# Kernel tuning notes

Hardware: AMD Instinct MI355X
Metric: run time of the kernel (lower is better)

The kernel has to match this reference:

```python
import jax, jax.numpy as jnp
import numpy as np
import math

B, S, D, H = 4, 2048, 512, 8
HD = D // H  # head dim = 64

def setup_inputs() -> dict:
    key = jax.random.key(0)
    ks = jax.random.split(key, 12)
    inp = {
        'queries': jax.random.normal(ks[0], (B, S, D), jnp.float32),
        'keys': jax.random.normal(ks[1], (B, S, D), jnp.float32),
        'values': jax.random.normal(ks[2], (B, S, D), jnp.float32),
        'valid_lens': jax.random.randint(ks[3], (B,), 0, 2048, jnp.int32),
        'Wq': jax.random.normal(ks[4], (D, D), jnp.float32) / math.sqrt(D),
        'bq': jnp.zeros((D,), jnp.float32),
        'Wk': jax.random.normal(ks[5], (D, D), jnp.float32) / math.sqrt(D),
        'bk': jnp.zeros((D,), jnp.float32),
        'Wv': jax.random.normal(ks[6], (D, D), jnp.float32) / math.sqrt(D),
        'bv': jnp.zeros((D,), jnp.float32),
        'Wo': jax.random.normal(ks[7], (D, D), jnp.float32) / math.sqrt(D),
        'bo': jnp.zeros((D,), jnp.float32),
    }
    return inp

def reference(queries, keys, values, valid_lens, Wq, bq, Wk, bk, Wv, bv, Wo, bo):
    # project and split heads: [B,S,D] -> [B,H,S,HD]
    def split_heads(x):
        return x.reshape(B, S, H, HD).transpose(0, 2, 1, 3)
    q = split_heads(queries @ Wq + bq)
    k = split_heads(keys @ Wk + bk)
    v = split_heads(values @ Wv + bv)
    # scores [B,H,Sq,Sk]
    scores = jnp.einsum('bhqd,bhkd->bhqk', q, k) / math.sqrt(HD)
    # masked softmax: mask key positions >= valid_len with -1e6 (d2l semantics)
    mask = jnp.arange(S)[None, None, None, :] < valid_lens[:, None, None, None]
    scores = jnp.where(mask, scores, -1e6)
    attn = jax.nn.softmax(scores, axis=-1)
    out = jnp.einsum('bhqk,bhkd->bhqd', attn, v)  # [B,H,S,HD]
    out = out.transpose(0, 2, 1, 3).reshape(B, S, D)
    return out @ Wo + bo
```

## Files before the change

### kernel.cpp

```cpp
#include <hip/hip_runtime.h>
#include <hip/hip_bf16.h>

typedef _Float16 half8 __attribute__((ext_vector_type(8)));
typedef _Float16 half4 __attribute__((ext_vector_type(4)));
typedef float floatx4 __attribute__((ext_vector_type(4)));

#define LOG2E 1.44269504088896340736f

__device__ __forceinline__ half8 cvt8(const float* p) {
    floatx4 a = *(const floatx4*)p;
    floatx4 b = *(const floatx4*)(p + 4);
    half8 h;
    h[0] = (_Float16)a[0]; h[1] = (_Float16)a[1]; h[2] = (_Float16)a[2]; h[3] = (_Float16)a[3];
    h[4] = (_Float16)b[0]; h[5] = (_Float16)b[1]; h[6] = (_Float16)b[2]; h[7] = (_Float16)b[3];
    return h;
}

__global__ __launch_bounds__(256) void transpose_w_kernel(
        const float* __restrict__ Wq, const float* __restrict__ Wk,
        const float* __restrict__ Wv, const float* __restrict__ Wo,
        _Float16* __restrict__ out) {
    const float* W = (blockIdx.z == 0) ? Wq : (blockIdx.z == 1) ? Wk : (blockIdx.z == 2) ? Wv : Wo;
    _Float16* o = out + (size_t)blockIdx.z * 512 * 512;
    __shared__ __align__(16) _Float16 t[64][72];
    int r0 = blockIdx.x * 64, c0 = blockIdx.y * 64;
    int tid = threadIdx.x;
    for (int i = 0; i < 2; i++) {
        int f = i * 256 + tid;
        int row = f >> 3, seg = f & 7;
        *(half8*)&t[row][seg * 8] = cvt8(W + (size_t)(r0 + row) * 512 + c0 + seg * 8);
    }
    __syncthreads();
    for (int i = 0; i < 2; i++) {
        int f = i * 256 + tid;
        int crow = f >> 3, seg = f & 7;
        half8 hv;
        for (int j = 0; j < 8; j++) hv[j] = t[seg * 8 + j][crow];
        *(half8*)(o + (size_t)(c0 + crow) * 512 + r0 + seg * 8) = hv;
    }
}

__global__ __launch_bounds__(256) void gemm_qkv_kernel(
        const float* __restrict__ Xq, const float* __restrict__ Xk, const float* __restrict__ Xv,
        const _Float16* __restrict__ WTall,
        const float* __restrict__ bq, const float* __restrict__ bk, const float* __restrict__ bv,
        _Float16* __restrict__ qo, _Float16* __restrict__ ko2, _Float16* __restrict__ vto) {
    int z = blockIdx.z;
    const float* X = (z == 0) ? Xq : (z == 1) ? Xk : Xv;
    const _Float16* BT = WTall + (size_t)z * 512 * 512;
    const float* bias = (z == 0) ? bq : (z == 1) ? bk : bv;

    __shared__ __align__(16) _Float16 Asm[128][72];
    __shared__ __align__(16) _Float16 Bsm[128][72];

    int tid = threadIdx.x;
    int wave = tid >> 6, lane = tid & 63;
    int lrow = lane & 15, quad = lane >> 4;
    int m0 = (wave >> 1) * 64, n0 = (wave & 1) * 64;
    int mBase = blockIdx.x * 128, nBase = blockIdx.y * 128;

    const floatx4 fz = {0.f, 0.f, 0.f, 0.f};
    floatx4 acc[4][4];
    for (int i = 0; i < 4; i++) for (int j = 0; j < 4; j++) acc[i][j] = fz;

    for (int kb = 0; kb < 512; kb += 64) {
        for (int i = 0; i < 4; i++) {
            int f = i * 256 + tid;
            int row = f >> 3, seg = f & 7;
            *(half8*)&Asm[row][seg * 8] = cvt8(X + (size_t)(mBase + row) * 512 + kb + seg * 8);
            *(half8*)&Bsm[row][seg * 8] = *(const half8*)(BT + (size_t)(nBase + row) * 512 + kb + seg * 8);
        }
        __syncthreads();
        for (int kc = 0; kc < 2; kc++) {
            int ko_ = kc * 32 + quad * 8;
            half8 a[4], b[4];
            for (int mt = 0; mt < 4; mt++) a[mt] = *(const half8*)&Asm[m0 + mt * 16 + lrow][ko_];
            for (int nt = 0; nt < 4; nt++) b[nt] = *(const half8*)&Bsm[n0 + nt * 16 + lrow][ko_];
            for (int mt = 0; mt < 4; mt++)
                for (int nt = 0; nt < 4; nt++)
                    acc[mt][nt] = __builtin_amdgcn_mfma_f32_16x16x32_f16(a[mt], b[nt], acc[mt][nt], 0, 0, 0);
        }
        __syncthreads();
    }

    if (z == 2) {
        for (int nt = 0; nt < 4; nt++) {
            int gc = nBase + n0 + nt * 16 + lrow;
            float bb = bias[gc];
            int h = gc >> 6, hd = gc & 63;
            for (int mt = 0; mt < 4; mt++) {
                int gr = mBase + m0 + mt * 16 + quad * 4;
                int b_ = gr >> 11, s = gr & 2047;
                half4 hv;
                for (int r = 0; r < 4; r++) hv[r] = (_Float16)(acc[mt][nt][r] + bb);
                *(half4*)(vto + (((size_t)(b_ * 8 + h) * 64 + hd) * 2048 + s)) = hv;
            }
        }
    } else {
        _Float16* out = (z == 0) ? qo : ko2;
        for (int nt = 0; nt < 4; nt++) {
            int gc = nBase + n0 + nt * 16 + lrow;
            float bb = bias[gc];
            int h = gc >> 6, hd = gc & 63;
            for (int mt = 0; mt < 4; mt++) {
                for (int r = 0; r < 4; r++) {
                    int gr = mBase + m0 + mt * 16 + quad * 4 + r;
                    int b_ = gr >> 11, s = gr & 2047;
                    out[(((size_t)b_ * 8 + h) * 2048 + s) * 64 + hd] = (_Float16)(acc[mt][nt][r] + bb);
                }
            }
        }
    }
}

__global__ __launch_bounds__(256) void attn_kernel(
        const _Float16* __restrict__ qws, const _Float16* __restrict__ kws, const _Float16* __restrict__ vtws,
        const int* __restrict__ vlens, _Float16* __restrict__ aout) {
    int idx = blockIdx.x;
    int b = ((idx & 3) + (idx >> 8)) & 3;
    int h = (idx >> 2) & 7;
    int q0 = ((idx >> 5) & 31) * 64;
    int bh = b * 8 + h;
    int L = vlens[b];
    bool uni = (L == 0);
    int nkt = uni ? 32 : ((L + 63) >> 6);
    int tid = threadIdx.x;
    int wave = tid >> 6, lane = tid & 63;
    int lrow = lane & 15, quad = lane >> 4;

    __shared__ __align__(16) _Float16 ksm[64][72];
    __shared__ __align__(16) _Float16 vtsm[80][72];

    for (int i = tid; i < 15 * 36; i += 256) {
        int r = i / 36, c = i % 36;
        ((float*)&vtsm[65 + r][0])[c] = 0.0f;
    }
    if (tid < 64) vtsm[64][tid] = (_Float16)1.0f;

    const _Float16* qbase = qws + ((size_t)bh * 2048 + q0) * 64;
    const _Float16* kbase = kws + (size_t)bh * 2048 * 64;
    const _Float16* vtbase = vtws + (size_t)bh * 64 * 2048;

    half8 qf[2];
    for (int kc = 0; kc < 2; kc++)
        qf[kc] = *(const half8*)(qbase + (wave * 16 + lrow) * 64 + kc * 32 + quad * 8);

    const floatx4 fz = {0.f, 0.f, 0.f, 0.f};
    floatx4 oacc[5];
    for (int nt = 0; nt < 5; nt++) oacc[nt] = fz;
    const float cexp = 0.125f * LOG2E;

    for (int kt = 0; kt < nkt; kt++) {
        const _Float16* ktile = kbase + (size_t)kt * 64 * 64;
        const _Float16* vttile = vtbase + kt * 64;
        for (int i = 0; i < 2; i++) {
            int f = i * 256 + tid;
            int row = f >> 3, seg = f & 7;
            *(half8*)&ksm[row][seg * 8] = *(const half8*)(ktile + f * 8);
            *(half8*)&vtsm[row][seg * 8] = *(const half8*)(vttile + (size_t)row * 2048 + seg * 8);
        }
        __syncthreads();

        floatx4 sacc[4];
        for (int km = 0; km < 4; km++) sacc[km] = fz;
        for (int kc = 0; kc < 2; kc++) {
            int ko_ = kc * 32 + quad * 8;
            for (int km = 0; km < 4; km++) {
                half8 kf = *(const half8*)&ksm[km * 16 + lrow][ko_];
                sacc[km] = __builtin_amdgcn_mfma_f32_16x16x32_f16(kf, qf[kc], sacc[km], 0, 0, 0);
            }
        }

        half4 pf[4];
        int kb0 = kt * 64 + quad * 4;
        for (int km = 0; km < 4; km++) {
            int kb = kb0 + km * 16;
            for (int r = 0; r < 4; r++) {
                float p = uni ? 1.0f : ((kb + r < L) ? exp2f(sacc[km][r] * cexp) : 0.0f);
                pf[km][r] = (_Float16)p;
            }
        }

        for (int km = 0; km < 4; km++) {
            int kk = km * 16 + quad * 4;
            for (int nt = 0; nt < 5; nt++) {
                half4 bvf = *(const half4*)&vtsm[nt * 16 + lrow][kk];
                oacc[nt] = __builtin_amdgcn_mfma_f32_16x16x16f16(pf[km], bvf, oacc[nt], 0, 0, 0);
            }
        }
        __syncthreads();
    }

    float inv[4];
    for (int r = 0; r < 4; r++)
        inv[r] = 1.0f / __shfl(oacc[4][r], quad << 4, 64);

    for (int nt = 0; nt < 4; nt++) {
        for (int r = 0; r < 4; r++) {
            int s = q0 + wave * 16 + quad * 4 + r;
            aout[((size_t)b * 2048 + s) * 512 + h * 64 + nt * 16 + lrow] =
                (_Float16)(oacc[nt][r] * inv[r]);
        }
    }
}

__global__ __launch_bounds__(256) void gemm_out_kernel(
        const _Float16* __restrict__ A, const _Float16* __restrict__ BT,
        const float* __restrict__ bias, float* __restrict__ out) {
    __shared__ __align__(16) _Float16 Asm[128][72];
    __shared__ __align__(16) _Float16 Bsm[128][72];

    int tid = threadIdx.x;
    int wave = tid >> 6, lane = tid & 63;
    int lrow = lane & 15, quad = lane >> 4;
    int m0 = (wave >> 1) * 64, n0 = (wave & 1) * 64;
    int mBase = blockIdx.x * 128, nBase = blockIdx.y * 128;

    const floatx4 fz = {0.f, 0.f, 0.f, 0.f};
    floatx4 acc[4][4];
    for (int i = 0; i < 4; i++) for (int j = 0; j < 4; j++) acc[i][j] = fz;

    for (int kb = 0; kb < 512; kb += 64) {
        for (int i = 0; i < 4; i++) {
            int f = i * 256 + tid;
            int row = f >> 3, seg = f & 7;
            *(half8*)&Asm[row][seg * 8] = *(const half8*)(A + (size_t)(mBase + row) * 512 + kb + seg * 8);
            *(half8*)&Bsm[row][seg * 8] = *(const half8*)(BT + (size_t)(nBase + row) * 512 + kb + seg * 8);
        }
        __syncthreads();
        for (int kc = 0; kc < 2; kc++) {
            int ko_ = kc * 32 + quad * 8;
            half8 a[4], b[4];
            for (int mt = 0; mt < 4; mt++) a[mt] = *(const half8*)&Asm[m0 + mt * 16 + lrow][ko_];
            for (int nt = 0; nt < 4; nt++) b[nt] = *(const half8*)&Bsm[n0 + nt * 16 + lrow][ko_];
            for (int mt = 0; mt < 4; mt++)
                for (int nt = 0; nt < 4; nt++)
                    acc[mt][nt] = __builtin_amdgcn_mfma_f32_16x16x32_f16(a[mt], b[nt], acc[mt][nt], 0, 0, 0);
        }
        __syncthreads();
    }

    for (int nt = 0; nt < 4; nt++) {
        int gc = nBase + n0 + nt * 16 + lrow;
        float bb = bias[gc];
        for (int mt = 0; mt < 4; mt++) {
            for (int r = 0; r < 4; r++) {
                int gr = mBase + m0 + mt * 16 + quad * 4 + r;
                out[(size_t)gr * 512 + gc] = acc[mt][nt][r] + bb;
            }
        }
    }
}

extern "C" void kernel_launch(void* const* d_in, const int* in_sizes, int n_in,
                              void* d_out, int out_size, void* d_ws, size_t ws_size,
                              hipStream_t stream) {
    const float* Q  = (const float*)d_in[0];
    const float* K  = (const float*)d_in[1];
    const float* V  = (const float*)d_in[2];
    const int*   VL = (const int*)d_in[3];
    const float* Wq = (const float*)d_in[4];
    const float* bq = (const float*)d_in[5];
    const float* Wk = (const float*)d_in[6];
    const float* bk = (const float*)d_in[7];
    const float* Wv = (const float*)d_in[8];
    const float* bv = (const float*)d_in[9];
    const float* Wo = (const float*)d_in[10];
    const float* bo = (const float*)d_in[11];

    char* ws = (char*)d_ws;
    _Float16* WT   = (_Float16*)ws;
    _Float16* qws  = (_Float16*)(ws + (size_t)(2)  * 1024 * 1024);
    _Float16* kws  = (_Float16*)(ws + (size_t)(10) * 1024 * 1024);
    _Float16* aout = (_Float16*)(ws + (size_t)(18) * 1024 * 1024);
    _Float16* vtws = (_Float16*)(ws + (size_t)(26) * 1024 * 1024);

    transpose_w_kernel<<<dim3(8, 8, 4), 256, 0, stream>>>(Wq, Wk, Wv, Wo, WT);
    gemm_qkv_kernel<<<dim3(64, 4, 3), 256, 0, stream>>>(Q, K, V, WT, bq, bk, bv, qws, kws, vtws);
    attn_kernel<<<dim3(1024, 1, 1), 256, 0, stream>>>(qws, kws, vtws, VL, aout);
    gemm_out_kernel<<<dim3(64, 4, 1), 256, 0, stream>>>(aout, WT + (size_t)3 * 512 * 512, bo, (float*)d_out);
}
```

Baseline: 206.9 us.

## Register-prefetch next tiles in GEMM and attention loops; fold softmax scale into Q

```diff
diff --git a/kernel.cpp b/kernel.cpp
--- a/kernel.cpp
+++ b/kernel.cpp
@@ -7,9 +7,7 @@
 
 #define LOG2E 1.44269504088896340736f
 
-__device__ __forceinline__ half8 cvt8(const float* p) {
-    floatx4 a = *(const floatx4*)p;
-    floatx4 b = *(const floatx4*)(p + 4);
+__device__ __forceinline__ half8 cvt8r(floatx4 a, floatx4 b) {
     half8 h;
     h[0] = (_Float16)a[0]; h[1] = (_Float16)a[1]; h[2] = (_Float16)a[2]; h[3] = (_Float16)a[3];
     h[4] = (_Float16)b[0]; h[5] = (_Float16)b[1]; h[6] = (_Float16)b[2]; h[7] = (_Float16)b[3];
@@ -28,7 +26,8 @@
     for (int i = 0; i < 2; i++) {
         int f = i * 256 + tid;
         int row = f >> 3, seg = f & 7;
-        *(half8*)&t[row][seg * 8] = cvt8(W + (size_t)(r0 + row) * 512 + c0 + seg * 8);
+        const float* p = W + (size_t)(r0 + row) * 512 + c0 + seg * 8;
+        *(half8*)&t[row][seg * 8] = cvt8r(*(const floatx4*)p, *(const floatx4*)(p + 4));
     }
     __syncthreads();
     for (int i = 0; i < 2; i++) {
@@ -63,14 +62,33 @@
     floatx4 acc[4][4];
     for (int i = 0; i < 4; i++) for (int j = 0; j < 4; j++) acc[i][j] = fz;
 
+    floatx4 areg[4][2];
+    half8 breg[4];
+    int srow[4], sseg[4];
+    for (int i = 0; i < 4; i++) { int f = i * 256 + tid; srow[i] = f >> 3; sseg[i] = f & 7; }
+
+    for (int i = 0; i < 4; i++) {
+        const float* pa = X + (size_t)(mBase + srow[i]) * 512 + sseg[i] * 8;
+        areg[i][0] = *(const floatx4*)pa;
+        areg[i][1] = *(const floatx4*)(pa + 4);
+        breg[i] = *(const half8*)(BT + (size_t)(nBase + srow[i]) * 512 + sseg[i] * 8);
+    }
+
     for (int kb = 0; kb < 512; kb += 64) {
         for (int i = 0; i < 4; i++) {
-            int f = i * 256 + tid;
-            int row = f >> 3, seg = f & 7;
-            *(half8*)&Asm[row][seg * 8] = cvt8(X + (size_t)(mBase + row) * 512 + kb + seg * 8);
-            *(half8*)&Bsm[row][seg * 8] = *(const half8*)(BT + (size_t)(nBase + row) * 512 + kb + seg * 8);
-        }
-        __syncthreads();
+            *(half8*)&Asm[srow[i]][sseg[i] * 8] = cvt8r(areg[i][0], areg[i][1]);
+            *(half8*)&Bsm[srow[i]][sseg[i] * 8] = breg[i];
+        }
+        __syncthreads();
+        if (kb + 64 < 512) {
+            int kn = kb + 64;
+            for (int i = 0; i < 4; i++) {
+                const float* pa = X + (size_t)(mBase + srow[i]) * 512 + kn + sseg[i] * 8;
+                areg[i][0] = *(const floatx4*)pa;
+                areg[i][1] = *(const floatx4*)(pa + 4);
+                breg[i] = *(const half8*)(BT + (size_t)(nBase + srow[i]) * 512 + kn + sseg[i] * 8);
+            }
+        }
         for (int kc = 0; kc < 2; kc++) {
             int ko_ = kc * 32 + quad * 8;
             half8 a[4], b[4];
@@ -142,24 +160,41 @@
     const _Float16* vtbase = vtws + (size_t)bh * 64 * 2048;
 
     half8 qf[2];
-    for (int kc = 0; kc < 2; kc++)
+    for (int kc = 0; kc < 2; kc++) {
         qf[kc] = *(const half8*)(qbase + (wave * 16 + lrow) * 64 + kc * 32 + quad * 8);
+        qf[kc] = qf[kc] * (_Float16)(0.125f * LOG2E);
+    }
 
     const floatx4 fz = {0.f, 0.f, 0.f, 0.f};
     floatx4 oacc[5];
     for (int nt = 0; nt < 5; nt++) oacc[nt] = fz;
-    const float cexp = 0.125f * LOG2E;
+
+    int row0 = tid >> 3, seg = tid & 7;
+    half8 kreg[2], vreg[2];
+    {
+        const _Float16* kt0 = kbase;
+        const _Float16* vt0 = vtbase;
+        kreg[0] = *(const half8*)(kt0 + tid * 8);
+        kreg[1] = *(const half8*)(kt0 + (256 + tid) * 8);
+        vreg[0] = *(const half8*)(vt0 + (size_t)row0 * 2048 + seg * 8);
+        vreg[1] = *(const half8*)(vt0 + (size_t)(row0 + 32) * 2048 + seg * 8);
+    }
 
     for (int kt = 0; kt < nkt; kt++) {
-        const _Float16* ktile = kbase + (size_t)kt * 64 * 64;
-        const _Float16* vttile = vtbase + kt * 64;
-        for (int i = 0; i < 2; i++) {
-            int f = i * 256 + tid;
-            int row = f >> 3, seg = f & 7;
-            *(half8*)&ksm[row][seg * 8] = *(const half8*)(ktile + f * 8);
-            *(half8*)&vtsm[row][seg * 8] = *(const half8*)(vttile + (size_t)row * 2048 + seg * 8);
-        }
-        __syncthreads();
+        *(half8*)&ksm[row0][seg * 8]        = kreg[0];
+        *(half8*)&ksm[row0 + 32][seg * 8]   = kreg[1];
+        *(half8*)&vtsm[row0][seg * 8]       = vreg[0];
+        *(half8*)&vtsm[row0 + 32][seg * 8]  = vreg[1];
+        __syncthreads();
+
+        if (kt + 1 < nkt) {
+            const _Float16* ktn = kbase + (size_t)(kt + 1) * 64 * 64;
+            const _Float16* vtn = vtbase + (kt + 1) * 64;
+            kreg[0] = *(const half8*)(ktn + tid * 8);
+            kreg[1] = *(const half8*)(ktn + (256 + tid) * 8);
+            vreg[0] = *(const half8*)(vtn + (size_t)row0 * 2048 + seg * 8);
+            vreg[1] = *(const half8*)(vtn + (size_t)(row0 + 32) * 2048 + seg * 8);
+        }
 
         floatx4 sacc[4];
         for (int km = 0; km < 4; km++) sacc[km] = fz;
@@ -176,7 +211,7 @@
         for (int km = 0; km < 4; km++) {
             int kb = kb0 + km * 16;
             for (int r = 0; r < 4; r++) {
-                float p = uni ? 1.0f : ((kb + r < L) ? exp2f(sacc[km][r] * cexp) : 0.0f);
+                float p = uni ? 1.0f : ((kb + r < L) ? exp2f(sacc[km][r]) : 0.0f);
                 pf[km][r] = (_Float16)p;
             }
         }
@@ -220,14 +255,27 @@
     floatx4 acc[4][4];
     for (int i = 0; i < 4; i++) for (int j = 0; j < 4; j++) acc[i][j] = fz;
 
+    half8 areg[4], breg[4];
+    int srow[4], sseg[4];
+    for (int i = 0; i < 4; i++) { int f = i * 256 + tid; srow[i] = f >> 3; sseg[i] = f & 7; }
+    for (int i = 0; i < 4; i++) {
+        areg[i] = *(const half8*)(A + (size_t)(mBase + srow[i]) * 512 + sseg[i] * 8);
+        breg[i] = *(const half8*)(BT + (size_t)(nBase + srow[i]) * 512 + sseg[i] * 8);
+    }
+
     for (int kb = 0; kb < 512; kb += 64) {
         for (int i = 0; i < 4; i++) {
-            int f = i * 256 + tid;
-            int row = f >> 3, seg = f & 7;
-            *(half8*)&Asm[row][seg * 8] = *(const half8*)(A + (size_t)(mBase + row) * 512 + kb + seg * 8);
-            *(half8*)&Bsm[row][seg * 8] = *(const half8*)(BT + (size_t)(nBase + row) * 512 + kb + seg * 8);
-        }
-        __syncthreads();
+            *(half8*)&Asm[srow[i]][sseg[i] * 8] = areg[i];
+            *(half8*)&Bsm[srow[i]][sseg[i] * 8] = breg[i];
+        }
+        __syncthreads();
+        if (kb + 64 < 512) {
+            int kn = kb + 64;
+            for (int i = 0; i < 4; i++) {
+                areg[i] = *(const half8*)(A + (size_t)(mBase + srow[i]) * 512 + kn + sseg[i] * 8);
+                breg[i] = *(const half8*)(BT + (size_t)(nBase + srow[i]) * 512 + kn + sseg[i] * 8);
+            }
+        }
         for (int kc = 0; kc < 2; kc++) {
             int ko_ = kc * 32 + quad * 8;
             half8 a[4], b[4];
```

After: 202.0 us. 1.02x faster.
